# Kernel tuning notes

Measured on AMD Instinct MI355X. Metric: run time of the kernel, lower is better.

The kernel has to match this reference:

```python
import jax, jax.numpy as jnp
import numpy as np

ALPHA = 0.2  # leaky relu slope
NEG_INF = -9e15

B, N, F_IN, F_OUT = 2, 4096, 256, 256
EMB = 16  # int(sqrt(256))


def setup_inputs() -> dict:
    key = jax.random.key(0)
    ks = jax.random.split(key, 16)
    g = 1.414

    def xavier(k, shape):
        fan_in, fan_out = shape[0], shape[1]
        limit = g * np.sqrt(6.0 / (fan_in + fan_out))
        return jax.random.uniform(k, shape, jnp.float32, -limit, limit)

    feat = jax.random.normal(ks[0], (B, N, F_IN), jnp.float32)
    adj = jax.random.randint(ks[1], (B, N, N), 0, 2, jnp.int32)
    W = xavier(ks[2], (F_IN, F_OUT))
    a1 = xavier(ks[3], (F_OUT, 1))
    a2 = xavier(ks[4], (F_OUT, 1))
    a12 = xavier(ks[5], (F_OUT, F_OUT))
    # BiInteraction linear layers stored as [in, out] (= torch weight.T)
    def lin(k1, k2, fi, fo):
        lim = 1.0 / np.sqrt(fi)
        w = jax.random.uniform(k1, (fi, fo), jnp.float32, -lim, lim)
        b = jax.random.uniform(k2, (fo,), jnp.float32, -lim, lim)
        return w, b

    e1_w, e1_b = lin(ks[6], ks[7], F_IN, EMB)
    e2_w, e2_b = lin(ks[8], ks[9], F_IN, EMB)
    i0_w, i0_b = lin(ks[10], ks[11], 2 * EMB, F_OUT)
    i1_w, i1_b = lin(ks[12], ks[13], F_OUT, F_OUT)
    return {"feat": feat, "adj": adj, "W": W, "a1": a1, "a2": a2,
            "a12": a12, "e1_w": e1_w, "e1_b": e1_b, "e2_w": e2_w,
            "e2_b": e2_b, "i0_w": i0_w, "i0_b": i0_b, "i1_w": i1_w,
            "i1_b": i1_b}


def reference(feat, adj, W, a1, a2, a12, e1_w, e1_b, e2_w, e2_b,
              i0_w, i0_b, i1_w, i1_b):
    lrelu = lambda x: jax.nn.leaky_relu(x, ALPHA)
    # attention scores: logits[b,i,j] = a1.h_j + a2.h_i + h_i A12 h_j
    h = feat @ W                                   # [B,N,F_OUT]
    Ax = (h @ a1).transpose(0, 2, 1)               # [B,1,N] (key term)
    Ay = h @ a2                                    # [B,N,1] (query term)
    Axy = jnp.einsum('bnd,de,bme->bnm', h, a12, h) # [B,N,N] bilinear
    e = lrelu(Ax + Ay + Axy)
    e = jnp.where(adj > 0, e, NEG_INF)
    attention = jax.nn.softmax(e, axis=-1)         # masked softmax over j
    h_prime = attention @ feat                     # [B,N,F_IN]
    # BiInteraction MLP update
    emb1 = lrelu(feat @ e1_w + e1_b)
    emb2 = lrelu(h_prime @ e2_w + e2_b)
    c = jnp.concatenate([emb1, emb2], axis=-1)     # [B,N,2*EMB]
    c = lrelu(c @ i0_w + i0_b)
    c = lrelu(c @ i1_w + i1_b)
    return c
```

## Files before the change

kernel.cpp:

```cpp
#include <hip/hip_runtime.h>
#include <hip/hip_bf16.h>

typedef __attribute__((ext_vector_type(8))) __bf16 bf16x8;
typedef __attribute__((ext_vector_type(8))) short short8;
typedef __attribute__((ext_vector_type(4))) float floatx4;
typedef __attribute__((ext_vector_type(4))) int intx4;
typedef unsigned short u16;
typedef unsigned int u32;
typedef unsigned long long u64;

constexpr int BB = 2, NN = 4096, DD = 256;
constexpr int NCHUNK = 4;
constexpr int KSTEP = 32;
constexpr int CHUNKLEN = NN / NCHUNK;
constexpr int STEPS = CHUNKLEN / KSTEP;
constexpr float SLOPE = 0.2f;
constexpr float NEGINF = -9e15f;

#define DEVI static __device__ __forceinline__

DEVI u16 f2bf(float f) {
  u32 u = __float_as_uint(f);
  u += 0x7fffu + ((u >> 16) & 1u);
  return (u16)(u >> 16);
}
DEVI float bf2f(u16 h) { return __uint_as_float(((u32)h) << 16); }
DEVI float lrelu(float x) { return x > 0.f ? x : SLOPE * x; }

DEVI floatx4 mfma16(short8 a, short8 b, floatx4 c) {
  return __builtin_amdgcn_mfma_f32_16x16x32_bf16(
      __builtin_bit_cast(bf16x8, a), __builtin_bit_cast(bf16x8, b), c, 0, 0, 0);
}

__global__ void k_prep_w(const float* W, const float* A12, const float* I1,
                         u16* WThi, u16* WTlo, u16* A12Thi, u16* A12Tlo,
                         u16* I1Thi, u16* I1Tlo) {
  __shared__ float tile[32][33];
  const float* src = blockIdx.z == 0 ? W : (blockIdx.z == 1 ? A12 : I1);
  u16* dhi = blockIdx.z == 0 ? WThi : (blockIdx.z == 1 ? A12Thi : I1Thi);
  u16* dlo = blockIdx.z == 0 ? WTlo : (blockIdx.z == 1 ? A12Tlo : I1Tlo);
  int k0 = blockIdx.x * 32, n0 = blockIdx.y * 32;
  int tx = threadIdx.x, ty = threadIdx.y;
  #pragma unroll
  for (int r = 0; r < 4; r++)
    tile[ty + r * 8][tx] = src[(size_t)(k0 + ty + r * 8) * 256 + n0 + tx];
  __syncthreads();
  #pragma unroll
  for (int r = 0; r < 4; r++) {
    float v = tile[tx][ty + r * 8];
    u16 hb = f2bf(v);
    size_t o = (size_t)(n0 + ty + r * 8) * 256 + k0 + tx;
    dhi[o] = hb;
    dlo[o] = f2bf(v - bf2f(hb));
  }
}

__global__ void k_adjpack(const int* adj, u64* maskp) {
  int wave = (blockIdx.x * 256 + threadIdx.x) >> 6;
  int lane = threadIdx.x & 63;
  size_t base = (size_t)wave * 256;
  const int* p = adj + base;
  u64 m[4];
  #pragma unroll
  for (int r = 0; r < 4; r++) {
    int v = p[r * 64 + lane];
    m[r] = __ballot(v > 0);
  }
  if (lane < 4) {
    u64 sel = lane == 0 ? m[0] : lane == 1 ? m[1] : lane == 2 ? m[2] : m[3];
    maskp[base / 64 + lane] = sel;
  }
}

template <int AMODE, int EPI>
__global__ __launch_bounds__(256) void k_gemm(
    const float* Af32, const u16* Ahi, const u16* Alo,
    const u16* BThi, const u16* BTlo,
    u16* Ohi, u16* Olo, float* Of32, const float* bias) {
  int t = threadIdx.x;
  int wid = t >> 6, lane = t & 63;
  int li = lane & 15, lg = lane >> 4;
  int row0 = blockIdx.x * 64 + wid * 16;
  int col0 = blockIdx.y * 32;
  int arow = row0 + li;

  __shared__ __align__(16) u16 Bh[32 * 256];
  __shared__ __align__(16) u16 Bl[32 * 256];
  #pragma unroll
  for (int s = 0; s < 4; s++) {
    int r = s * 8 + (t >> 5), c8 = (t & 31) * 8;
    int off = r * 256 + (c8 ^ ((r & 7) << 3));
    *(intx4*)(Bh + off) = *(const intx4*)(BThi + (size_t)(col0 + r) * DD + c8);
    *(intx4*)(Bl + off) = *(const intx4*)(BTlo + (size_t)(col0 + r) * DD + c8);
  }

  short8 ahi[8], alo[8];
  if constexpr (AMODE == 0) {
    const float* ap = Af32 + (size_t)arow * DD + lg * 8;
    #pragma unroll
    for (int ks = 0; ks < 8; ks++) {
      floatx4 f0 = *(const floatx4*)(ap + ks * 32);
      floatx4 f1 = *(const floatx4*)(ap + ks * 32 + 4);
      short8 h, l;
      #pragma unroll
      for (int e = 0; e < 4; e++) {
        u16 hb = f2bf(f0[e]); h[e] = (short)hb; l[e] = (short)f2bf(f0[e] - bf2f(hb));
        u16 hb2 = f2bf(f1[e]); h[e + 4] = (short)hb2; l[e + 4] = (short)f2bf(f1[e] - bf2f(hb2));
      }
      ahi[ks] = h; alo[ks] = l;
    }
  } else {
    const u16* ap = Ahi + (size_t)arow * DD + lg * 8;
    const u16* ap2 = Alo + (size_t)arow * DD + lg * 8;
    #pragma unroll
    for (int ks = 0; ks < 8; ks++) {
      ahi[ks] = *(const short8*)(ap + ks * 32);
      alo[ks] = *(const short8*)(ap2 + ks * 32);
    }
  }
  __syncthreads();

  floatx4 acc[2];
  #pragma unroll
  for (int cf = 0; cf < 2; cf++) acc[cf] = 0.f;

  #pragma unroll
  for (int cf = 0; cf < 2; cf++) {
    int row = cf * 16 + li;
    int rsw = (row & 7) << 3;
    #pragma unroll
    for (int ks = 0; ks < 8; ks++) {
      int off = row * 256 + ((ks * 32 + lg * 8) ^ rsw);
      short8 bhf = *(const short8*)(Bh + off);
      short8 blf = *(const short8*)(Bl + off);
      acc[cf] = mfma16(ahi[ks], bhf, acc[cf]);
      acc[cf] = mfma16(alo[ks], bhf, acc[cf]);
      acc[cf] = mfma16(ahi[ks], blf, acc[cf]);
    }
  }

  #pragma unroll
  for (int cf = 0; cf < 2; cf++) {
    int col = col0 + cf * 16 + li;
    #pragma unroll
    for (int r = 0; r < 4; r++) {
      int row = row0 + lg * 4 + r;
      float v = acc[cf][r];
      if constexpr (EPI == 0) {
        u16 hb = f2bf(v);
        Ohi[(size_t)row * DD + col] = hb;
        Olo[(size_t)row * DD + col] = f2bf(v - bf2f(hb));
      } else {
        v += bias[col];
        v = lrelu(v);
        Of32[(size_t)row * DD + col] = v;
      }
    }
  }
}

__global__ void k_axay(const u16* h_hi, const u16* h_lo, const float* a1,
                       const float* a2, float* ax, float* ay) {
  int row = blockIdx.x * 4 + (threadIdx.x >> 6);
  int lane = threadIdx.x & 63;
  const u16* ph = h_hi + (size_t)row * DD + lane * 4;
  const u16* pl = h_lo + (size_t)row * DD + lane * 4;
  float s1 = 0.f, s2 = 0.f;
  #pragma unroll
  for (int r = 0; r < 4; r++) {
    float hv = bf2f(ph[r]) + bf2f(pl[r]);
    s1 += hv * a1[lane * 4 + r];
    s2 += hv * a2[lane * 4 + r];
  }
  #pragma unroll
  for (int off = 32; off; off >>= 1) {
    s1 += __shfl_xor(s1, off);
    s2 += __shfl_xor(s2, off);
  }
  if (lane == 0) { ax[row] = s1; ay[row] = s2; }
}

__global__ void k_featT(const float* feat, u16* featT) {
  __shared__ float tile[64][65];
  int b = blockIdx.z, n0 = blockIdx.x * 64, d0 = blockIdx.y * 64;
  int tx = threadIdx.x & 63, ty = threadIdx.x >> 6;
  #pragma unroll
  for (int r = 0; r < 16; r++) {
    int n = ty + r * 4;
    tile[n][tx] = feat[((size_t)b * NN + n0 + n) * DD + d0 + tx];
  }
  __syncthreads();
  #pragma unroll
  for (int r = 0; r < 16; r++) {
    int d = ty + r * 4;
    featT[((size_t)b * DD + d0 + d) * NN + n0 + tx] = f2bf(tile[tx][d]);
  }
}

__global__ __launch_bounds__(256, 2) void k_flash(
    const u16* t_hi, const u16* t_lo, const u16* h_hi, const u16* h_lo,
    const u16* featT, const float* ax, const float* ay, const u64* maskp,
    float* PO, float* m_ws, float* l_ws) {
  int b = blockIdx.z, chunk = blockIdx.y, it = blockIdx.x;
  int t = threadIdx.x;
  int wid = t >> 6, lane = t & 63;
  int li = lane & 15, lg = lane >> 4;
  int i = it * 64 + wid * 16 + li;
  size_t browQ = (size_t)b * NN + i;

  __shared__ __align__(16) u16 Kh[KSTEP * 256];
  __shared__ __align__(16) u16 Kl[KSTEP * 256];
  __shared__ __align__(16) u16 Vs[256 * KSTEP];
  __shared__ __align__(16) u16 Pbuf[4][16][40];

  short8 qhi[8], qlo[8];
  {
    const u16* qp = t_hi + browQ * DD + lg * 8;
    const u16* qp2 = t_lo + browQ * DD + lg * 8;
    #pragma unroll
    for (int ks = 0; ks < 8; ks++) {
      qhi[ks] = *(const short8*)(qp + ks * 32);
      qlo[ks] = *(const short8*)(qp2 + ks * 32);
    }
  }
  float ayv = ay[browQ];
  const float* axp = ax + (size_t)b * NN;
  const u32* mrow = (const u32*)maskp + browQ * (NN / 32);
  const u16* kh_src = h_hi + ((size_t)b * NN + chunk * CHUNKLEN) * DD;
  const u16* kl_src = h_lo + ((size_t)b * NN + chunk * CHUNKLEN) * DD;
  const u16* v_src = featT + (size_t)b * DD * NN + chunk * CHUNKLEN;

  floatx4 acc[16];
  #pragma unroll
  for (int df = 0; df < 16; df++) acc[df] = 0.f;
  float m_run = -INFINITY, l_run = 0.f;

  intx4 sKh[4], sKl[4], sVv[4];
  {
    int r = (t >> 5), c8 = (t & 31) * 8;
    int dv = (t >> 2), cv = (t & 3) * 8;
    #pragma unroll
    for (int s = 0; s < 4; s++) {
      sKh[s] = *(const intx4*)(kh_src + (size_t)(s * 8 + r) * DD + c8);
      sKl[s] = *(const intx4*)(kl_src + (size_t)(s * 8 + r) * DD + c8);
      sVv[s] = *(const intx4*)(v_src + (size_t)(s * 64 + dv) * NN + cv);
    }
  }

  for (int jt = 0; jt < STEPS; jt++) {
    __syncthreads();
    {
      int r0 = (t >> 5), c8 = (t & 31) * 8;
      int dv0 = (t >> 2), cv = (t & 3) * 8;
      #pragma unroll
      for (int s = 0; s < 4; s++) {
        int r = s * 8 + r0;
        int off = r * 256 + (c8 ^ ((r & 7) << 3));
        *(intx4*)(Kh + off) = sKh[s];
        *(intx4*)(Kl + off) = sKl[s];
        int d = s * 64 + dv0;
        *(intx4*)(Vs + d * KSTEP + (cv ^ (((d >> 1) & 3) << 3))) = sVv[s];
      }
    }
    __syncthreads();
    int j0 = jt * KSTEP;
    if (jt + 1 < STEPS) {
      const u16* kh2 = kh_src + (size_t)(j0 + KSTEP) * DD;
      const u16* kl2 = kl_src + (size_t)(j0 + KSTEP) * DD;
      int r = (t >> 5), c8 = (t & 31) * 8;
      int dv = (t >> 2), cv = (t & 3) * 8;
      #pragma unroll
      for (int s = 0; s < 4; s++) {
        sKh[s] = *(const intx4*)(kh2 + (size_t)(s * 8 + r) * DD + c8);
        sKl[s] = *(const intx4*)(kl2 + (size_t)(s * 8 + r) * DD + c8);
        sVv[s] = *(const intx4*)(v_src + (size_t)(s * 64 + dv) * NN + (j0 + KSTEP) + cv);
      }
    }

    int ja = chunk * CHUNKLEN + j0;
    u32 M = mrow[ja >> 5];
    floatx4 axv[2];
    axv[0] = *(const floatx4*)(axp + ja + lg * 4);
    axv[1] = *(const floatx4*)(axp + ja + 16 + lg * 4);

    floatx4 sacc[2];
    sacc[0] = 0.f; sacc[1] = 0.f;
    #pragma unroll
    for (int ks = 0; ks < 8; ks++) {
      #pragma unroll
      for (int fi = 0; fi < 2; fi++) {
        int row = fi * 16 + li;
        int off = row * 256 + ((ks * 32 + lg * 8) ^ ((row & 7) << 3));
        short8 a0 = *(const short8*)(Kh + off);
        short8 a1 = *(const short8*)(Kl + off);
        sacc[fi] = mfma16(a0, qhi[ks], sacc[fi]);
        sacc[fi] = mfma16(a1, qhi[ks], sacc[fi]);
        sacc[fi] = mfma16(a0, qlo[ks], sacc[fi]);
      }
    }
    float sv[2][4];
    float m_tile = -INFINITY;
    #pragma unroll
    for (int fi = 0; fi < 2; fi++) {
      u32 nib = (M >> (fi * 16 + lg * 4)) & 0xFu;
      #pragma unroll
      for (int r = 0; r < 4; r++) {
        float s = sacc[fi][r] + axv[fi][r] + ayv;
        s = lrelu(s);
        s = (nib >> r) & 1u ? s : NEGINF;
        sv[fi][r] = s;
        m_tile = fmaxf(m_tile, s);
      }
    }
    m_tile = fmaxf(m_tile, __shfl_xor(m_tile, 16));
    m_tile = fmaxf(m_tile, __shfl_xor(m_tile, 32));
    bool nores = __all(m_tile <= m_run);
    if (!nores) {
      float m_new = fmaxf(m_run, m_tile);
      float scale = __expf(m_run - m_new);
      l_run *= scale;
      #pragma unroll
      for (int df = 0; df < 16; df++) acc[df] *= scale;
      m_run = m_new;
    }

    float psum = 0.f;
    #pragma unroll
    for (int fi = 0; fi < 2; fi++) {
      u16 pb[4];
      #pragma unroll
      for (int r = 0; r < 4; r++) {
        float p = __expf(sv[fi][r] - m_run);
        pb[r] = f2bf(p);
        psum += bf2f(pb[r]);
      }
      u32 w0 = (u32)pb[0] | ((u32)pb[1] << 16);
      u32 w1 = (u32)pb[2] | ((u32)pb[3] << 16);
      *(uint2*)&Pbuf[wid][li][fi * 16 + lg * 4] = make_uint2(w0, w1);
    }
    psum += __shfl_xor(psum, 16);
    psum += __shfl_xor(psum, 32);
    l_run += psum;

    short8 pf = *(const short8*)&Pbuf[wid][li][lg * 8];
    #pragma unroll
    for (int df = 0; df < 16; df++) {
      int d = df * 16 + li;
      short8 vf = *(const short8*)(Vs + d * KSTEP + ((lg * 8) ^ (((d >> 1) & 3) << 3)));
      acc[df] = mfma16(vf, pf, acc[df]);
    }
  }

  size_t pobase = ((size_t)(b * NCHUNK + chunk) * NN + i) * DD;
  #pragma unroll
  for (int df = 0; df < 16; df++)
    *(floatx4*)(PO + pobase + df * 16 + lg * 4) = acc[df];
  if (lg == 0) {
    size_t mi = ((size_t)b * NCHUNK + chunk) * NN + i;
    m_ws[mi] = m_run;
    l_ws[mi] = l_run;
  }
}

__global__ void k_combine(const float* PO, const float* m_ws, const float* l_ws,
                          float* h_prime) {
  int b = blockIdx.y;
  int t = threadIdx.x;
  int i = blockIdx.x * 4 + (t >> 6);
  int d4 = (t & 63) * 4;
  float mc[NCHUNK], lc[NCHUNK];
  #pragma unroll
  for (int c = 0; c < NCHUNK; c++) {
    mc[c] = m_ws[((size_t)b * NCHUNK + c) * NN + i];
    lc[c] = l_ws[((size_t)b * NCHUNK + c) * NN + i];
  }
  float M = -INFINITY;
  #pragma unroll
  for (int c = 0; c < NCHUNK; c++) M = fmaxf(M, mc[c]);
  float w[NCHUNK], L = 0.f;
  #pragma unroll
  for (int c = 0; c < NCHUNK; c++) { w[c] = __expf(mc[c] - M); L += w[c] * lc[c]; }
  float invL = 1.f / L;

  floatx4 s = 0.f;
  #pragma unroll
  for (int c = 0; c < NCHUNK; c++) {
    floatx4 v = *(const floatx4*)(PO + ((size_t)(b * NCHUNK + c) * NN + i) * DD + d4);
    s += w[c] * v;
  }
  *(floatx4*)(h_prime + ((size_t)b * NN + i) * DD + d4) = s * invL;
}

__global__ void k_mlp(const float* feat, const float* h_prime,
                      const float* e1w, const float* e1b, const float* e2w,
                      const float* e2b, const float* i0w, const float* i0b,
                      u16* c_hi, u16* c_lo) {
  int row = blockIdx.x * 4 + (threadIdx.x >> 6);
  int lane = threadIdx.x & 63;
  floatx4 fv = *(const floatx4*)(feat + (size_t)row * DD + lane * 4);
  floatx4 hv = *(const floatx4*)(h_prime + (size_t)row * DD + lane * 4);
  float p1[16], p2[16];
  #pragma unroll
  for (int o = 0; o < 16; o++) { p1[o] = 0.f; p2[o] = 0.f; }
  #pragma unroll
  for (int r = 0; r < 4; r++) {
    int d = lane * 4 + r;
    const float* w1 = e1w + (size_t)d * 16;
    const float* w2 = e2w + (size_t)d * 16;
    #pragma unroll
    for (int o = 0; o < 16; o++) {
      p1[o] += fv[r] * w1[o];
      p2[o] += hv[r] * w2[o];
    }
  }
  #pragma unroll
  for (int off = 32; off; off >>= 1) {
    #pragma unroll
    for (int o = 0; o < 16; o++) {
      p1[o] += __shfl_xor(p1[o], off);
      p2[o] += __shfl_xor(p2[o], off);
    }
  }
  float cc[32];
  #pragma unroll
  for (int o = 0; o < 16; o++) {
    cc[o] = lrelu(p1[o] + e1b[o]);
    cc[16 + o] = lrelu(p2[o] + e2b[o]);
  }
  #pragma unroll
  for (int q = 0; q < 4; q++) {
    int o2 = q * 64 + lane;
    float s = i0b[o2];
    #pragma unroll
    for (int k = 0; k < 32; k++) s += cc[k] * i0w[(size_t)k * 256 + o2];
    s = lrelu(s);
    u16 hb = f2bf(s);
    c_hi[(size_t)row * DD + o2] = hb;
    c_lo[(size_t)row * DD + o2] = f2bf(s - bf2f(hb));
  }
}

extern "C" void kernel_launch(void* const* d_in, const int* in_sizes, int n_in,
                              void* d_out, int out_size, void* d_ws,
                              size_t ws_size, hipStream_t stream) {
  const float* feat = (const float*)d_in[0];
  const int* adj = (const int*)d_in[1];
  const float* W = (const float*)d_in[2];
  const float* a1 = (const float*)d_in[3];
  const float* a2 = (const float*)d_in[4];
  const float* a12 = (const float*)d_in[5];
  const float* e1w = (const float*)d_in[6];
  const float* e1b = (const float*)d_in[7];
  const float* e2w = (const float*)d_in[8];
  const float* e2b = (const float*)d_in[9];
  const float* i0w = (const float*)d_in[10];
  const float* i0b = (const float*)d_in[11];
  const float* i1w = (const float*)d_in[12];
  const float* i1b = (const float*)d_in[13];
  float* out = (float*)d_out;

  char* p = (char*)d_ws;
  auto carve = [&](size_t bytes) -> char* {
    char* r = p;
    p += (bytes + 255) & ~(size_t)255;
    return r;
  };
  const size_t MAT = 256 * 256 * sizeof(u16);
  const size_t BND = (size_t)BB * NN * DD * sizeof(u16);
  u16* WThi = (u16*)carve(MAT);
  u16* WTlo = (u16*)carve(MAT);
  u16* A12Thi = (u16*)carve(MAT);
  u16* A12Tlo = (u16*)carve(MAT);
  u16* I1Thi = (u16*)carve(MAT);
  u16* I1Tlo = (u16*)carve(MAT);
  u16* h_hi = (u16*)carve(BND);
  u16* h_lo = (u16*)carve(BND);
  u16* t_hi = (u16*)carve(BND);
  u16* t_lo = (u16*)carve(BND);
  u16* featT = (u16*)carve(BND);
  float* ax = (float*)carve((size_t)BB * NN * 4);
  float* ay = (float*)carve((size_t)BB * NN * 4);
  u64* maskp = (u64*)carve((size_t)BB * NN * (NN / 64) * 8);
  float* PO = (float*)carve((size_t)BB * NCHUNK * NN * DD * 4);
  float* m_ws = (float*)carve((size_t)BB * NCHUNK * NN * 4);
  float* l_ws = (float*)carve((size_t)BB * NCHUNK * NN * 4);
  float* h_prime = (float*)carve((size_t)BB * NN * DD * 4);
  u16* c_hi = (u16*)carve(BND);
  u16* c_lo = (u16*)carve(BND);

  k_adjpack<<<32768, 256, 0, stream>>>(adj, maskp);
  k_prep_w<<<dim3(8, 8, 3), dim3(32, 8), 0, stream>>>(
      W, a12, i1w, WThi, WTlo, A12Thi, A12Tlo, I1Thi, I1Tlo);
  k_gemm<0, 0><<<dim3(128, 8), 256, 0, stream>>>(
      feat, nullptr, nullptr, WThi, WTlo, h_hi, h_lo, nullptr, nullptr);
  k_axay<<<2048, 256, 0, stream>>>(h_hi, h_lo, a1, a2, ax, ay);
  k_gemm<1, 0><<<dim3(128, 8), 256, 0, stream>>>(
      nullptr, h_hi, h_lo, A12Thi, A12Tlo, t_hi, t_lo, nullptr, nullptr);
  k_featT<<<dim3(64, 4, 2), 256, 0, stream>>>(feat, featT);
  k_flash<<<dim3(64, NCHUNK, 2), 256, 0, stream>>>(
      t_hi, t_lo, h_hi, h_lo, featT, ax, ay, maskp, PO, m_ws, l_ws);
  k_combine<<<dim3(1024, 2), 256, 0, stream>>>(PO, m_ws, l_ws, h_prime);
  k_mlp<<<2048, 256, 0, stream>>>(feat, h_prime, e1w, e1b, e2w, e2b, i0w, i0b,
                                  c_hi, c_lo);
  k_gemm<1, 1><<<dim3(128, 8), 256, 0, stream>>>(
      nullptr, c_hi, c_lo, I1Thi, I1Tlo, nullptr, nullptr, out, i1b);
}
```

Measured before the change: 428.0 us.

## Fuse split-K combine into MLP, double flash chunks, vectorize axay loads

Measured after the change: 421.9 us. No clear change (-1.4%).

```diff
diff --git a/kernel.cpp b/kernel.cpp
--- a/kernel.cpp
+++ b/kernel.cpp
@@ -10,7 +10,7 @@
 typedef unsigned long long u64;
 
 constexpr int BB = 2, NN = 4096, DD = 256;
-constexpr int NCHUNK = 4;
+constexpr int NCHUNK = 8;
 constexpr int KSTEP = 32;
 constexpr int CHUNKLEN = NN / NCHUNK;
 constexpr int STEPS = CHUNKLEN / KSTEP;
@@ -163,14 +163,18 @@
                        const float* a2, float* ax, float* ay) {
   int row = blockIdx.x * 4 + (threadIdx.x >> 6);
   int lane = threadIdx.x & 63;
-  const u16* ph = h_hi + (size_t)row * DD + lane * 4;
-  const u16* pl = h_lo + (size_t)row * DD + lane * 4;
+  ushort4 hw = *(const ushort4*)(h_hi + (size_t)row * DD + lane * 4);
+  ushort4 lw = *(const ushort4*)(h_lo + (size_t)row * DD + lane * 4);
+  floatx4 av1 = *(const floatx4*)(a1 + lane * 4);
+  floatx4 av2 = *(const floatx4*)(a2 + lane * 4);
+  const u16* hp = (const u16*)&hw;
+  const u16* lp = (const u16*)&lw;
   float s1 = 0.f, s2 = 0.f;
   #pragma unroll
   for (int r = 0; r < 4; r++) {
-    float hv = bf2f(ph[r]) + bf2f(pl[r]);
-    s1 += hv * a1[lane * 4 + r];
-    s2 += hv * a2[lane * 4 + r];
+    float hv = bf2f(hp[r]) + bf2f(lp[r]);
+    s1 += hv * av1[r];
+    s2 += hv * av2[r];
   }
   #pragma unroll
   for (int off = 32; off; off >>= 1) {
@@ -362,12 +366,19 @@
   }
 }
 
-__global__ void k_combine(const float* PO, const float* m_ws, const float* l_ws,
-                          float* h_prime) {
+__global__ void k_combine_mlp(const float* PO, const float* m_ws,
+                              const float* l_ws, const float* feat,
+                              const float* e1w, const float* e1b,
+                              const float* e2w, const float* e2b,
+                              const float* i0w, const float* i0b,
+                              u16* c_hi, u16* c_lo) {
   int b = blockIdx.y;
   int t = threadIdx.x;
   int i = blockIdx.x * 4 + (t >> 6);
-  int d4 = (t & 63) * 4;
+  int lane = t & 63;
+  int d4 = lane * 4;
+  size_t row = (size_t)b * NN + i;
+
   float mc[NCHUNK], lc[NCHUNK];
   #pragma unroll
   for (int c = 0; c < NCHUNK; c++) {
@@ -382,29 +393,21 @@
   for (int c = 0; c < NCHUNK; c++) { w[c] = __expf(mc[c] - M); L += w[c] * lc[c]; }
   float invL = 1.f / L;
 
-  floatx4 s = 0.f;
+  floatx4 hv = 0.f;
   #pragma unroll
   for (int c = 0; c < NCHUNK; c++) {
     floatx4 v = *(const floatx4*)(PO + ((size_t)(b * NCHUNK + c) * NN + i) * DD + d4);
-    s += w[c] * v;
-  }
-  *(floatx4*)(h_prime + ((size_t)b * NN + i) * DD + d4) = s * invL;
-}
-
-__global__ void k_mlp(const float* feat, const float* h_prime,
-                      const float* e1w, const float* e1b, const float* e2w,
-                      const float* e2b, const float* i0w, const float* i0b,
-                      u16* c_hi, u16* c_lo) {
-  int row = blockIdx.x * 4 + (threadIdx.x >> 6);
-  int lane = threadIdx.x & 63;
-  floatx4 fv = *(const floatx4*)(feat + (size_t)row * DD + lane * 4);
-  floatx4 hv = *(const floatx4*)(h_prime + (size_t)row * DD + lane * 4);
+    hv += w[c] * v;
+  }
+  hv *= invL;
+
+  floatx4 fv = *(const floatx4*)(feat + row * DD + d4);
   float p1[16], p2[16];
   #pragma unroll
   for (int o = 0; o < 16; o++) { p1[o] = 0.f; p2[o] = 0.f; }
   #pragma unroll
   for (int r = 0; r < 4; r++) {
-    int d = lane * 4 + r;
+    int d = d4 + r;
     const float* w1 = e1w + (size_t)d * 16;
     const float* w2 = e2w + (size_t)d * 16;
     #pragma unroll
@@ -435,8 +438,8 @@
     for (int k = 0; k < 32; k++) s += cc[k] * i0w[(size_t)k * 256 + o2];
     s = lrelu(s);
     u16 hb = f2bf(s);
-    c_hi[(size_t)row * DD + o2] = hb;
-    c_lo[(size_t)row * DD + o2] = f2bf(s - bf2f(hb));
+    c_hi[row * DD + o2] = hb;
+    c_lo[row * DD + o2] = f2bf(s - bf2f(hb));
   }
 }
 
@@ -484,7 +487,6 @@
   float* PO = (float*)carve((size_t)BB * NCHUNK * NN * DD * 4);
   float* m_ws = (float*)carve((size_t)BB * NCHUNK * NN * 4);
   float* l_ws = (float*)carve((size_t)BB * NCHUNK * NN * 4);
-  float* h_prime = (float*)carve((size_t)BB * NN * DD * 4);
   u16* c_hi = (u16*)carve(BND);
   u16* c_lo = (u16*)carve(BND);
 
@@ -499,9 +501,8 @@
   k_featT<<<dim3(64, 4, 2), 256, 0, stream>>>(feat, featT);
   k_flash<<<dim3(64, NCHUNK, 2), 256, 0, stream>>>(
       t_hi, t_lo, h_hi, h_lo, featT, ax, ay, maskp, PO, m_ws, l_ws);
-  k_combine<<<dim3(1024, 2), 256, 0, stream>>>(PO, m_ws, l_ws, h_prime);
-  k_mlp<<<2048, 256, 0, stream>>>(feat, h_prime, e1w, e1b, e2w, e2b, i0w, i0b,
-                                  c_hi, c_lo);
+  k_combine_mlp<<<dim3(1024, 2), 256, 0, stream>>>(
+      PO, m_ws, l_ws, feat, e1w, e1b, e2w, e2b, i0w, i0b, c_hi, c_lo);
   k_gemm<1, 1><<<dim3(128, 8), 256, 0, stream>>>(
       nullptr, c_hi, c_lo, I1Thi, I1Tlo, nullptr, nullptr, out, i1b);
 }
```
